# Kernel optimization log

Measured on AMD Instinct MI355X. Metric: run time of the kernel, lower is better.

## Reference

```python
import jax, jax.numpy as jnp
import numpy as np

N, E, IN, H, D = 50000, 800000, 256, 4, 32
NEG_SLOPE = 0.2


def setup_inputs() -> dict:
    key = jax.random.key(0)
    ks = jax.random.split(key, 11)
    feat = jax.random.normal(ks[0], (N, IN), jnp.float32)
    src = jax.random.randint(ks[1], (E,), 0, N, jnp.int32)
    dst = jax.random.randint(ks[2], (E,), 0, N, jnp.int32)
    # ppmi in [1, 10) so log(log(ppmi)) path is non-trivial
    ppmi = 1.0 + 9.0 * jax.random.uniform(ks[3], (E,), jnp.float32)
    eps_src = jax.random.normal(ks[4], (N, H, 1), jnp.float32)
    eps_dst = jax.random.normal(ks[5], (N, H, 1), jnp.float32)
    W = jax.random.normal(ks[6], (IN, H * D), jnp.float32) * (1.0 / np.sqrt(IN))
    mu_src = jax.random.normal(ks[7], (1, H, D), jnp.float32) * 0.02
    mu_dst = jax.random.normal(ks[8], (1, H, D), jnp.float32) * 0.02
    lam_src = jax.random.normal(ks[9], (1, H, D), jnp.float32) * 0.02
    lam_dst = jax.random.normal(ks[10], (1, H, D), jnp.float32) * 0.02
    return dict(feat=feat, src=src, dst=dst, ppmi=ppmi, eps_src=eps_src,
                eps_dst=eps_dst, W=W, mu_src=mu_src, mu_dst=mu_dst,
                lam_src=lam_src, lam_dst=lam_dst)


def reference(feat, src, dst, ppmi, eps_src, eps_dst, W, mu_src, mu_dst, lam_src, lam_dst):
    n = feat.shape[0]
    h, d = mu_src.shape[1], mu_src.shape[2]
    ft = (feat @ W).reshape(n, h, d)                      # [N,H,D]
    # per-node attention scalars (src == dst node set here)
    mu_s = (ft * mu_src).sum(-1, keepdims=True)           # [N,H,1]
    lam_s = (ft * lam_src).sum(-1, keepdims=True)
    mu_d = (ft * mu_dst).sum(-1, keepdims=True)
    lam_d = (ft * lam_src).sum(-1, keepdims=True)         # original uses lam_src here (replicated)
    # reparameterize z = eps * exp(0.5*logvar) + mu
    z_src = eps_src * jnp.exp(0.5 * lam_s) + mu_s
    z_dst = eps_dst * jnp.exp(0.5 * lam_d) + mu_d
    e = jax.nn.leaky_relu(z_src[src] + z_dst[dst], NEG_SLOPE)   # [E,H,1]
    scale = jnp.clip(jnp.log(jnp.clip(jnp.log(ppmi), 1.0, None)), 1.0, None)
    e2 = e * scale[:, None, None]
    # edge softmax over destination segments
    emax = jax.ops.segment_max(e2, dst, num_segments=n)   # [N,H,1]
    ee = jnp.exp(e2 - emax[dst])
    denom = jax.ops.segment_sum(ee, dst, num_segments=n)
    a = ee / denom[dst]                                    # [E,H,1]
    # weighted scatter-sum aggregation: u_mul_e + sum
    rst = jax.ops.segment_sum(ft[src] * a, dst, num_segments=n)  # [N,H,D]
    return rst, mu_s + mu_d, lam_s + lam_d
```

## Files before the change

### kernel.cpp

```cpp
#include <hip/hip_runtime.h>

#define N_NODES 50000
#define N_EDGES 800000
#define IN_DIM  256
#define NH      4
#define HD      128
#define NEG_SLOPE 0.2f
#define SCAN_BLOCKS ((N_NODES + 255) / 256)
#define HIST_BLOCKS ((N_EDGES + 255) / 256)
#define WT_BLOCKS   ((HD * IN_DIM) / 256)
#define K1B_BLOCKS  ((N_NODES * NH + 255) / 256)

typedef short          v8s __attribute__((ext_vector_type(8)));
typedef float          v4f __attribute__((ext_vector_type(4)));
typedef unsigned short us8 __attribute__((ext_vector_type(8)));

__device__ __forceinline__ unsigned short f2bf(float f)
{
    unsigned int u = __float_as_uint(f);
    u += 0x7fffu + ((u >> 16) & 1u);
    return (unsigned short)(u >> 16);
}
__device__ __forceinline__ float bf2f(unsigned int bits16)
{
    return __uint_as_float(bits16 << 16);
}

__device__ __forceinline__ float edge_scale(float p)
{
    const float lp = fmaxf(__logf(p), 1.0f);
    return fmaxf(__logf(lp), 1.0f);
}

__global__ __launch_bounds__(256) void k_wt_hist(
    const float* __restrict__ W, unsigned short* __restrict__ Wt_bf,
    const int* __restrict__ dst, int* __restrict__ counts)
{
    const int b = blockIdx.x;
    if (b < HIST_BLOCKS) {
        const int e = b * 256 + threadIdx.x;
        if (e < N_EDGES) atomicAdd(&counts[dst[e]], 1);
    } else {
        const int idx = (b - HIST_BLOCKS) * 256 + threadIdx.x;
        const int n = idx >> 8;
        const int k = idx & 255;
        Wt_bf[n * IN_DIM + k] = f2bf(W[(size_t)k * HD + n]);
    }
}

#define AS 40
#define CS 136

__global__ __launch_bounds__(256) void k1_mfma(
    const float* __restrict__ feat, const unsigned short* __restrict__ Wt_bf,
    unsigned short* __restrict__ ft_bf)
{
    __shared__ ushort smem[17408];
    ushort* A_sh = smem;
    ushort* B_sh = smem + 128 * AS;

    const int t    = threadIdx.x;
    const int lane = t & 63;
    const int wv   = t >> 6;
    const int r0   = blockIdx.x * 128;

    const int arow = t >> 3;
    const int akk  = (t & 7) * 4;
    int rA[4];
#pragma unroll
    for (int p = 0; p < 4; ++p) rA[p] = min(r0 + arow + 32 * p, N_NODES - 1);
    const int bn  = t >> 2;
    const int bk8 = (t & 3) * 8;

    float4 fa[4];
    us8    fb[2];

#define LOADC(kc0)                                                              \
    do {                                                                        \
        _Pragma("unroll")                                                       \
        for (int p = 0; p < 4; ++p)                                             \
            fa[p] = *(const float4*)(feat + (size_t)rA[p] * IN_DIM + (kc0) + akk); \
        _Pragma("unroll")                                                       \
        for (int p = 0; p < 2; ++p)                                             \
            fb[p] = *(const us8*)(Wt_bf + (size_t)(bn + 64 * p) * IN_DIM + (kc0) + bk8); \
    } while (0)

    v4f acc[2][8];
#pragma unroll
    for (int i = 0; i < 2; ++i)
#pragma unroll
        for (int j = 0; j < 8; ++j) acc[i][j] = (v4f)(0.0f);

    const int frow = lane & 15;
    const int fq   = lane >> 4;

    LOADC(0);

    for (int c = 0; c < IN_DIM / 32; ++c) {
        __syncthreads();
#pragma unroll
        for (int p = 0; p < 4; ++p) {
            ushort4 u;
            u.x = f2bf(fa[p].x); u.y = f2bf(fa[p].y);
            u.z = f2bf(fa[p].z); u.w = f2bf(fa[p].w);
            *(ushort4*)(A_sh + (arow + 32 * p) * AS + akk) = u;
        }
#pragma unroll
        for (int p = 0; p < 2; ++p)
            *(us8*)(B_sh + (bn + 64 * p) * AS + bk8) = fb[p];
        __syncthreads();

        if (c + 1 < IN_DIM / 32) LOADC((c + 1) * 32);

        v8s a0 = *(const v8s*)(A_sh + (wv * 32 + frow) * AS + fq * 8);
        v8s a1 = *(const v8s*)(A_sh + (wv * 32 + 16 + frow) * AS + fq * 8);
        v8s bfr[8];
#pragma unroll
        for (int nf = 0; nf < 8; ++nf)
            bfr[nf] = *(const v8s*)(B_sh + (nf * 16 + frow) * AS + fq * 8);
#pragma unroll
        for (int nf = 0; nf < 8; ++nf) {
            acc[0][nf] = __builtin_amdgcn_mfma_f32_16x16x32_bf16(
                a0, bfr[nf], acc[0][nf], 0, 0, 0);
            acc[1][nf] = __builtin_amdgcn_mfma_f32_16x16x32_bf16(
                a1, bfr[nf], acc[1][nf], 0, 0, 0);
        }
    }

    __syncthreads();
    ushort* Cw = smem + wv * (32 * CS);
#pragma unroll
    for (int mf = 0; mf < 2; ++mf)
#pragma unroll
        for (int nf = 0; nf < 8; ++nf)
#pragma unroll
            for (int r = 0; r < 4; ++r)
                Cw[(mf * 16 + fq * 4 + r) * CS + nf * 16 + frow] =
                    f2bf(acc[mf][nf][r]);
    __syncthreads();

#pragma unroll
    for (int p = 0; p < 8; ++p) {
        const int row_l = (lane >> 4) + 4 * p;
        const int colv  = (lane & 15) * 8;
        const us8 val = *(const us8*)(Cw + row_l * CS + colv);
        const int grow = r0 + wv * 32 + row_l;
        if (grow < N_NODES)
            *(us8*)(ft_bf + (size_t)grow * HD + colv) = val;
    }
}

__global__ __launch_bounds__(256) void k_k1b_scanlocal(
    const int* __restrict__ counts, int* __restrict__ local,
    int* __restrict__ bsums,
    const unsigned short* __restrict__ ft_bf,
    const float* __restrict__ mu_src, const float* __restrict__ mu_dst,
    const float* __restrict__ lam_src,
    const float* __restrict__ eps_src, const float* __restrict__ eps_dst,
    float* __restrict__ z_src_ws, float* __restrict__ z_dst_ws,
    float* __restrict__ mu_out, float* __restrict__ lam_out)
{
    __shared__ int sh[256];
    const int b = blockIdx.x;
    const int t = threadIdx.x;

    if (b < SCAN_BLOCKS) {
        const int i = b * 256 + t;
        const int v = (i < N_NODES) ? counts[i] : 0;
        sh[t] = v;
        __syncthreads();
#pragma unroll
        for (int off = 1; off < 256; off <<= 1) {
            int x = (t >= off) ? sh[t - off] : 0;
            __syncthreads();
            sh[t] += x;
            __syncthreads();
        }
        if (i < N_NODES) local[i] = sh[t] - v;
        if (t == 255) bsums[b] = sh[255];
        return;
    }

    const int g = (b - SCAN_BLOCKS) * 256 + t;
    if (g >= N_NODES * NH) return;
    const int row = g >> 2;
    const int h   = g & 3;

    const unsigned short* fr = ft_bf + (size_t)row * HD + h * 32;
    const float* ms = mu_src + h * 32;
    const float* md = mu_dst + h * 32;
    const float* ls = lam_src + h * 32;

    float pm = 0.0f, pd = 0.0f, pl = 0.0f;
#pragma unroll
    for (int v = 0; v < 4; ++v) {
        const us8 u = *(const us8*)(fr + v * 8);
#pragma unroll
        for (int j = 0; j < 8; ++j) {
            const float f = bf2f(u[j]);
            const int   i = v * 8 + j;
            pm = fmaf(f, ms[i], pm);
            pd = fmaf(f, md[i], pd);
            pl = fmaf(f, ls[i], pl);
        }
    }
    const float sdev = expf(0.5f * pl);
    z_src_ws[g] = eps_src[g] * sdev + pm;
    z_dst_ws[g] = eps_dst[g] * sdev + pd;
    mu_out[g]   = pm + pd;
    lam_out[g]  = 2.0f * pl;
}

__global__ __launch_bounds__(256) void k_scan_bsums(
    const int* __restrict__ bsums, int* __restrict__ bscan)
{
    __shared__ int sh[256];
    const int t = threadIdx.x;
    const int v = (t < SCAN_BLOCKS) ? bsums[t] : 0;
    sh[t] = v;
    __syncthreads();
#pragma unroll
    for (int off = 1; off < 256; off <<= 1) {
        int x = (t >= off) ? sh[t - off] : 0;
        __syncthreads();
        sh[t] += x;
        __syncthreads();
    }
    if (t < SCAN_BLOCKS) bscan[t] = sh[t] - v;
}

__global__ __launch_bounds__(256) void k_scan_add(
    const int* __restrict__ local, const int* __restrict__ bscan,
    int* __restrict__ offsets, int* __restrict__ cursor)
{
    const int i = blockIdx.x * 256 + threadIdx.x;
    if (i >= N_NODES) return;
    const int o = local[i] + bscan[blockIdx.x];
    offsets[i] = o;
    cursor[i]  = o;
}

__global__ __launch_bounds__(256) void k_scatter(
    const int* __restrict__ src, const int* __restrict__ dst,
    const float* __restrict__ ppmi,
    int* __restrict__ cursor, int2* __restrict__ rec_sorted)
{
    const int e = blockIdx.x * 256 + threadIdx.x;
    if (e >= N_EDGES) return;
    const int s  = src[e];
    const int d0 = dst[e];
    const int j  = atomicAdd(&cursor[d0], 1);
    rec_sorted[j] = make_int2(s, __float_as_int(edge_scale(ppmi[e])));
}

__device__ __forceinline__ float edge_w1(float zs, float zd, float sc)
{
    float v = zs + zd;
    v = (v >= 0.0f) ? v : NEG_SLOPE * v;
    return __expf(v * sc);
}

__global__ __launch_bounds__(64) void k3_csr(
    const int* __restrict__ offsets, const int* __restrict__ counts,
    const int2* __restrict__ rec_sorted,
    const float* __restrict__ z_src_ws, const float* __restrict__ z_dst_ws,
    const unsigned int* __restrict__ ft_u32, float2* __restrict__ rst2)
{
    const int node = blockIdx.x;
    const int lane = threadIdx.x;
    const int h    = lane >> 4;
    const int start = offsets[node];
    const int deg   = counts[node];
    const float zd  = z_dst_ws[node * NH + h];

    float ax = 0.0f, ay = 0.0f, wsum = 0.0f;

    int i = 0;
    for (; i + 4 <= deg; i += 4) {
        const int2 r0 = rec_sorted[start + i];
        const int2 r1 = rec_sorted[start + i + 1];
        const int2 r2 = rec_sorted[start + i + 2];
        const int2 r3 = rec_sorted[start + i + 3];
        const float z0 = z_src_ws[r0.x * NH + h];
        const float z1 = z_src_ws[r1.x * NH + h];
        const float z2 = z_src_ws[r2.x * NH + h];
        const float z3 = z_src_ws[r3.x * NH + h];
        const unsigned f0 = ft_u32[(size_t)r0.x * (HD / 2) + lane];
        const unsigned f1 = ft_u32[(size_t)r1.x * (HD / 2) + lane];
        const unsigned f2 = ft_u32[(size_t)r2.x * (HD / 2) + lane];
        const unsigned f3 = ft_u32[(size_t)r3.x * (HD / 2) + lane];
        const float w0 = edge_w1(z0, zd, __int_as_float(r0.y));
        const float w1 = edge_w1(z1, zd, __int_as_float(r1.y));
        const float w2 = edge_w1(z2, zd, __int_as_float(r2.y));
        const float w3 = edge_w1(z3, zd, __int_as_float(r3.y));
        ax = fmaf(bf2f(f0 & 0xffffu), w0, ax);
        ay = fmaf(bf2f(f0 >> 16),     w0, ay);
        ax = fmaf(bf2f(f1 & 0xffffu), w1, ax);
        ay = fmaf(bf2f(f1 >> 16),     w1, ay);
        ax = fmaf(bf2f(f2 & 0xffffu), w2, ax);
        ay = fmaf(bf2f(f2 >> 16),     w2, ay);
        ax = fmaf(bf2f(f3 & 0xffffu), w3, ax);
        ay = fmaf(bf2f(f3 >> 16),     w3, ay);
        wsum += (w0 + w1) + (w2 + w3);
    }
    for (; i < deg; ++i) {
        const int2 r0 = rec_sorted[start + i];
        const float z0 = z_src_ws[r0.x * NH + h];
        const unsigned f0 = ft_u32[(size_t)r0.x * (HD / 2) + lane];
        const float w0 = edge_w1(z0, zd, __int_as_float(r0.y));
        ax = fmaf(bf2f(f0 & 0xffffu), w0, ax);
        ay = fmaf(bf2f(f0 >> 16),     w0, ay);
        wsum += w0;
    }

    const float inv = (wsum > 0.0f) ? 1.0f / wsum : 0.0f;
    rst2[(size_t)node * (HD / 2) + lane] = make_float2(ax * inv, ay * inv);
}

extern "C" void kernel_launch(void* const* d_in, const int* in_sizes, int n_in,
                              void* d_out, int out_size, void* d_ws, size_t ws_size,
                              hipStream_t stream)
{
    const float* feat    = (const float*)d_in[0];
    const int*   src     = (const int*)  d_in[1];
    const int*   dst     = (const int*)  d_in[2];
    const float* ppmi    = (const float*)d_in[3];
    const float* eps_src = (const float*)d_in[4];
    const float* eps_dst = (const float*)d_in[5];
    const float* W       = (const float*)d_in[6];
    const float* mu_src  = (const float*)d_in[7];
    const float* mu_dst  = (const float*)d_in[8];
    const float* lam_src = (const float*)d_in[9];

    float* out     = (float*)d_out;
    float* rst     = out;
    float* mu_out  = out + (size_t)N_NODES * HD;
    float* lam_out = mu_out + (size_t)N_NODES * NH;

    char* wsb = (char*)d_ws;
    int2*           rec_s  = (int2*)wsb;
    unsigned short* ft_bf  = (unsigned short*)(wsb + (size_t)N_EDGES * 8);
    unsigned short* Wt_bf  = ft_bf + (size_t)N_NODES * HD;
    float*          zs_ws  = (float*)(Wt_bf + (size_t)HD * IN_DIM);
    float*          zd_ws  = zs_ws + (size_t)N_NODES * NH;
    int*            counts = (int*)(zd_ws + (size_t)N_NODES * NH);
    int*            local  = counts + N_NODES;
    int*            offsets= local + N_NODES;
    int*            cursor = offsets + N_NODES;
    int*            bsums  = cursor + N_NODES;
    int*            bscan  = bsums + 256;

    hipMemsetAsync(counts, 0, N_NODES * sizeof(int), stream);

    k_wt_hist<<<HIST_BLOCKS + WT_BLOCKS, 256, 0, stream>>>(
        W, Wt_bf, dst, counts);

    k1_mfma<<<(N_NODES + 127) / 128, 256, 0, stream>>>(feat, Wt_bf, ft_bf);

    k_k1b_scanlocal<<<SCAN_BLOCKS + K1B_BLOCKS, 256, 0, stream>>>(
        counts, local, bsums,
        ft_bf, mu_src, mu_dst, lam_src, eps_src, eps_dst,
        zs_ws, zd_ws, mu_out, lam_out);

    k_scan_bsums<<<1, 256, 0, stream>>>(bsums, bscan);
    k_scan_add<<<SCAN_BLOCKS, 256, 0, stream>>>(local, bscan, offsets, cursor);

    k_scatter<<<HIST_BLOCKS, 256, 0, stream>>>(src, dst, ppmi, cursor, rec_s);

    k3_csr<<<N_NODES, 64, 0, stream>>>(
        offsets, counts, rec_s, zs_ws, zd_ws,
        (const unsigned int*)ft_bf, (float2*)rst);
}
```

Measured before the change: 258.0 us.

## Reuse histogram atomic ranks for scatter and pad edge records with nontemporal access

The histogram pass now keeps the return value of each atomic increment as the edge's rank within its destination segment. The scatter kernel then computes positions as offset plus rank, which removes the second pass of atomics and the cursor array. Edge records are also padded from 8 to 16 bytes and written and read with nontemporal builtins. This costs an extra rank array and doubles the record traffic, in exchange for removing contended atomics from the scatter.

```diff
diff --git a/kernel.cpp b/kernel.cpp
--- a/kernel.cpp
+++ b/kernel.cpp
@@ -14,6 +14,7 @@
 typedef short          v8s __attribute__((ext_vector_type(8)));
 typedef float          v4f __attribute__((ext_vector_type(4)));
 typedef unsigned short us8 __attribute__((ext_vector_type(8)));
+typedef int            v4i __attribute__((ext_vector_type(4)));
 
 __device__ __forceinline__ unsigned short f2bf(float f)
 {
@@ -34,12 +35,13 @@
 
 __global__ __launch_bounds__(256) void k_wt_hist(
     const float* __restrict__ W, unsigned short* __restrict__ Wt_bf,
-    const int* __restrict__ dst, int* __restrict__ counts)
+    const int* __restrict__ dst, int* __restrict__ counts,
+    int* __restrict__ rank)
 {
     const int b = blockIdx.x;
     if (b < HIST_BLOCKS) {
         const int e = b * 256 + threadIdx.x;
-        if (e < N_EDGES) atomicAdd(&counts[dst[e]], 1);
+        if (e < N_EDGES) rank[e] = atomicAdd(&counts[dst[e]], 1);
     } else {
         const int idx = (b - HIST_BLOCKS) * 256 + threadIdx.x;
         const int n = idx >> 8;
@@ -231,26 +233,28 @@
 
 __global__ __launch_bounds__(256) void k_scan_add(
     const int* __restrict__ local, const int* __restrict__ bscan,
-    int* __restrict__ offsets, int* __restrict__ cursor)
+    int* __restrict__ offsets)
 {
     const int i = blockIdx.x * 256 + threadIdx.x;
     if (i >= N_NODES) return;
-    const int o = local[i] + bscan[blockIdx.x];
-    offsets[i] = o;
-    cursor[i]  = o;
+    offsets[i] = local[i] + bscan[blockIdx.x];
 }
 
 __global__ __launch_bounds__(256) void k_scatter(
     const int* __restrict__ src, const int* __restrict__ dst,
-    const float* __restrict__ ppmi,
-    int* __restrict__ cursor, int2* __restrict__ rec_sorted)
+    const float* __restrict__ ppmi, const int* __restrict__ rank,
+    const int* __restrict__ offsets, v4i* __restrict__ rec_sorted)
 {
     const int e = blockIdx.x * 256 + threadIdx.x;
     if (e >= N_EDGES) return;
-    const int s  = src[e];
     const int d0 = dst[e];
-    const int j  = atomicAdd(&cursor[d0], 1);
-    rec_sorted[j] = make_int2(s, __float_as_int(edge_scale(ppmi[e])));
+    const int j  = offsets[d0] + rank[e];
+    v4i rec;
+    rec.x = src[e];
+    rec.y = __float_as_int(edge_scale(ppmi[e]));
+    rec.z = 0;
+    rec.w = 0;
+    __builtin_nontemporal_store(rec, rec_sorted + j);
 }
 
 __device__ __forceinline__ float edge_w1(float zs, float zd, float sc)
@@ -262,7 +266,7 @@
 
 __global__ __launch_bounds__(64) void k3_csr(
     const int* __restrict__ offsets, const int* __restrict__ counts,
-    const int2* __restrict__ rec_sorted,
+    const v4i* __restrict__ rec_sorted,
     const float* __restrict__ z_src_ws, const float* __restrict__ z_dst_ws,
     const unsigned int* __restrict__ ft_u32, float2* __restrict__ rst2)
 {
@@ -277,10 +281,10 @@
 
     int i = 0;
     for (; i + 4 <= deg; i += 4) {
-        const int2 r0 = rec_sorted[start + i];
-        const int2 r1 = rec_sorted[start + i + 1];
-        const int2 r2 = rec_sorted[start + i + 2];
-        const int2 r3 = rec_sorted[start + i + 3];
+        const v4i r0 = __builtin_nontemporal_load(rec_sorted + start + i);
+        const v4i r1 = __builtin_nontemporal_load(rec_sorted + start + i + 1);
+        const v4i r2 = __builtin_nontemporal_load(rec_sorted + start + i + 2);
+        const v4i r3 = __builtin_nontemporal_load(rec_sorted + start + i + 3);
         const float z0 = z_src_ws[r0.x * NH + h];
         const float z1 = z_src_ws[r1.x * NH + h];
         const float z2 = z_src_ws[r2.x * NH + h];
@@ -304,7 +308,7 @@
         wsum += (w0 + w1) + (w2 + w3);
     }
     for (; i < deg; ++i) {
-        const int2 r0 = rec_sorted[start + i];
+        const v4i r0 = __builtin_nontemporal_load(rec_sorted + start + i);
         const float z0 = z_src_ws[r0.x * NH + h];
         const unsigned f0 = ft_u32[(size_t)r0.x * (HD / 2) + lane];
         const float w0 = edge_w1(z0, zd, __int_as_float(r0.y));
@@ -338,22 +342,22 @@
     float* lam_out = mu_out + (size_t)N_NODES * NH;
 
     char* wsb = (char*)d_ws;
-    int2*           rec_s  = (int2*)wsb;
-    unsigned short* ft_bf  = (unsigned short*)(wsb + (size_t)N_EDGES * 8);
+    v4i*            rec_s  = (v4i*)wsb;
+    unsigned short* ft_bf  = (unsigned short*)(wsb + (size_t)N_EDGES * 16);
     unsigned short* Wt_bf  = ft_bf + (size_t)N_NODES * HD;
     float*          zs_ws  = (float*)(Wt_bf + (size_t)HD * IN_DIM);
     float*          zd_ws  = zs_ws + (size_t)N_NODES * NH;
     int*            counts = (int*)(zd_ws + (size_t)N_NODES * NH);
     int*            local  = counts + N_NODES;
     int*            offsets= local + N_NODES;
-    int*            cursor = offsets + N_NODES;
-    int*            bsums  = cursor + N_NODES;
+    int*            bsums  = offsets + N_NODES;
     int*            bscan  = bsums + 256;
+    int*            rank   = bscan + 256;
 
     hipMemsetAsync(counts, 0, N_NODES * sizeof(int), stream);
 
     k_wt_hist<<<HIST_BLOCKS + WT_BLOCKS, 256, 0, stream>>>(
-        W, Wt_bf, dst, counts);
+        W, Wt_bf, dst, counts, rank);
 
     k1_mfma<<<(N_NODES + 127) / 128, 256, 0, stream>>>(feat, Wt_bf, ft_bf);
 
@@ -363,9 +367,10 @@
         zs_ws, zd_ws, mu_out, lam_out);
 
     k_scan_bsums<<<1, 256, 0, stream>>>(bsums, bscan);
-    k_scan_add<<<SCAN_BLOCKS, 256, 0, stream>>>(local, bscan, offsets, cursor);
-
-    k_scatter<<<HIST_BLOCKS, 256, 0, stream>>>(src, dst, ppmi, cursor, rec_s);
+    k_scan_add<<<SCAN_BLOCKS, 256, 0, stream>>>(local, bscan, offsets);
+
+    k_scatter<<<HIST_BLOCKS, 256, 0, stream>>>(
+        src, dst, ppmi, rank, offsets, rec_s);
 
     k3_csr<<<N_NODES, 64, 0, stream>>>(
         offsets, counts, rec_s, zs_ws, zd_ws,
```

Result: faster. 240.1 us (-6.9%).
